# Performance work log

Measured on AMD Instinct MI355X. Metric: run time of the kernel, lower is better.

Reference implementation:

```python
import jax, jax.numpy as jnp
import numpy as np

B, N, K, H = 4, 2048, 30, 128
NODE_IN, EDGE_IN, FF = 21, 16, 4 * H


def _normalize(t, axis=-1):
    d = t / jnp.linalg.norm(t, axis=axis, keepdims=True)
    return jnp.where(jnp.isnan(d), 0.0, d)


def gather_nodes(nodes, idx):
    # nodes: [B,N,C], idx: [B,N,K] -> [B,N,K,C]
    b, n, k = idx.shape
    flat = idx.reshape(b, n * k)
    out = jnp.take_along_axis(nodes, flat[:, :, None], axis=1)
    return out.reshape(b, n, k, nodes.shape[-1])


def cal_dihedral(Xf, eps=1e-7):
    dX = Xf[:, 1:, :] - Xf[:, :-1, :]
    U = _normalize(dX)
    u0, u1, u2 = U[:, :-2], U[:, 1:-1], U[:, 2:]
    n0 = _normalize(jnp.cross(u0, u1))
    n1 = _normalize(jnp.cross(u1, u2))
    cosD = jnp.clip((n0 * n1).sum(-1), -1 + eps, 1 - eps)
    v = _normalize(jnp.cross(n0, n1))
    return jnp.sign((-v * u1).sum(-1)) * jnp.arccos(cosD)


def dihedrals(X, eps=1e-7):
    b, n = X.shape[0], X.shape[1]
    Xf = X[:, :, :3, :].reshape(b, 3 * n, 3)
    D = cal_dihedral(Xf)
    D = jnp.pad(D, ((0, 0), (1, 2))).reshape(b, n, 3)
    dihed = jnp.concatenate([jnp.cos(D), jnp.sin(D)], -1)
    dX = Xf[:, 1:] - Xf[:, :-1]
    U = _normalize(dX)
    cosA = jnp.clip((U[:, :-2] * U[:, 1:-1]).sum(-1), -1 + eps, 1 - eps)
    A = jnp.pad(jnp.arccos(cosA), ((0, 0), (1, 2))).reshape(b, n, 3)
    ang = jnp.concatenate([jnp.cos(A), jnp.sin(A)], -1)
    return jnp.concatenate([dihed, ang], -1)  # [B,N,12]


def quaternions(R):
    diag = jnp.diagonal(R, axis1=-2, axis2=-1)
    Rxx, Ryy, Rzz = diag[..., 0], diag[..., 1], diag[..., 2]
    mags = 0.5 * jnp.sqrt(jnp.abs(1 + jnp.stack([Rxx - Ryy - Rzz, -Rxx + Ryy - Rzz, -Rxx - Ryy + Rzz], -1)))
    signs = jnp.sign(jnp.stack([R[..., 2, 1] - R[..., 1, 2], R[..., 0, 2] - R[..., 2, 0], R[..., 1, 0] - R[..., 0, 1]], -1))
    xyz = signs * mags
    w = jnp.sqrt(jax.nn.relu(1 + diag.sum(-1, keepdims=True))) / 2.0
    return _normalize(jnp.concatenate([xyz, w], -1))


def orientations(X, E_idx):
    V = X  # [B,N,4,3]
    b, n = X.shape[0], X.shape[1]
    k = E_idx.shape[2]
    Xf = X[:, :, :3, :].reshape(b, 3 * n, 3)
    dX = Xf[:, 1:] - Xf[:, :-1]
    U = _normalize(dX)
    u0, u1 = U[:, :-2], U[:, 1:-1]
    n0 = _normalize(jnp.cross(u0, u1))[:, ::3]
    b1 = _normalize(u0 - u1)[:, ::3]
    Xa = Xf[:, ::3]  # [B,N,3]
    Q = jnp.stack([b1, n0, jnp.cross(b1, n0)], 2)  # [B,N-1,3,3]
    Q = Q.reshape(b, Q.shape[1], 9)
    Q = jnp.pad(Q, ((0, 0), (0, 1), (0, 0)))  # [B,N,9]
    Qn = gather_nodes(Q, E_idx).reshape(b, n, k, 3, 3)
    Xn = gather_nodes(V[:, :, 1, :], E_idx)
    Nn = gather_nodes(V[:, :, 0, :], E_idx)
    Cn = gather_nodes(V[:, :, 2, :], E_idx)
    On = gather_nodes(V[:, :, 3, :], E_idx)
    Q3 = Q.reshape(b, n, 3, 3)
    dXn = jnp.stack([Xn, Nn, Cn, On], 3) - Xa[:, :, None, None, :]  # [B,N,K,4,3]
    dU = jnp.einsum('bnij,bnkaj->bnkai', Q3, dXn)
    E_direct = _normalize(dU).reshape(b, n, k, 12)
    R = jnp.einsum('bnji,bnkjl->bnkil', Q3, Qn)  # Q^T @ Q_neighbors
    q = quaternions(R)  # [B,N,K,4]
    dX_inner = V[:, :, jnp.array([0, 2, 3]), :] - Xa[:, :, None, :]
    dU_inner = _normalize(jnp.einsum('bnij,bnaj->bnai', Q3, dX_inner))
    V_direct = dU_inner.reshape(b, n, 9)
    return V_direct, E_direct, q


def layernorm(x, g, bta, eps=1e-5):
    m = x.mean(-1, keepdims=True)
    v = ((x - m) ** 2).mean(-1, keepdims=True)
    return (x - m) / jnp.sqrt(v + eps) * g + bta


def gelu(x):
    return jax.nn.gelu(x, approximate=False)


def forward(X, E_idx, Wv_w, Wv_b, We_w, We_b, W1_w, W1_b, W2_w, W2_b, W3_w, W3_b,
            Wi_w, Wi_b, Wo_w, Wo_b, ln1_g, ln1_b, ln2_g, ln2_b):
    k = E_idx.shape[2]
    Dfeat = dihedrals(X)                     # [B,N,12]
    Vd, Ed, q = orientations(X, E_idx)       # [B,N,9],[B,N,K,12],[B,N,K,4]
    hV = jnp.concatenate([Dfeat, Vd], -1) @ Wv_w + Wv_b     # [B,N,H]
    hE = jnp.concatenate([Ed, q], -1) @ We_w + We_b         # [B,N,K,H]
    hV_nbr = gather_nodes(hV, E_idx)                        # [B,N,K,H]
    hV_exp = jnp.broadcast_to(hV[:, :, None, :], hV_nbr.shape)
    hEV = jnp.concatenate([hV_exp, hE, hV_nbr], -1)         # [B,N,K,3H]
    msg = gelu(hEV @ W1_w + W1_b)
    msg = gelu(msg @ W2_w + W2_b)
    msg = msg @ W3_w + W3_b
    dh = msg.sum(-2) / k
    hV = layernorm(hV + dh, ln1_g, ln1_b)
    ff = gelu(hV @ Wi_w + Wi_b) @ Wo_w + Wo_b
    hV = layernorm(hV + ff, ln2_g, ln2_b)
    return hV


def _lin(key, fan_in, fan_out):
    s = 1.0 / np.sqrt(fan_in)
    kw, kb = jax.random.split(key)
    return (jax.random.uniform(kw, (fan_in, fan_out), minval=-s, maxval=s),
            jax.random.uniform(kb, (fan_out,), minval=-s, maxval=s))


def setup_inputs() -> dict:
    key = jax.random.key(0)
    ks = jax.random.split(key, 10)
    X = jax.random.normal(ks[0], (B, N, 4, 3), dtype=jnp.float32) * 3.0
    E_idx = jax.random.randint(ks[1], (B, N, K), 0, N)
    Wv_w, Wv_b = _lin(ks[2], NODE_IN, H)
    We_w, We_b = _lin(ks[3], EDGE_IN, H)
    W1_w, W1_b = _lin(ks[4], 3 * H, H)
    W2_w, W2_b = _lin(ks[5], H, H)
    W3_w, W3_b = _lin(ks[6], H, H)
    Wi_w, Wi_b = _lin(ks[7], H, FF)
    Wo_w, Wo_b = _lin(ks[8], FF, H)
    return {
        'X': X, 'E_idx': E_idx,
        'Wv_w': Wv_w, 'Wv_b': Wv_b, 'We_w': We_w, 'We_b': We_b,
        'W1_w': W1_w, 'W1_b': W1_b, 'W2_w': W2_w, 'W2_b': W2_b,
        'W3_w': W3_w, 'W3_b': W3_b, 'Wi_w': Wi_w, 'Wi_b': Wi_b,
        'Wo_w': Wo_w, 'Wo_b': Wo_b,
        'ln1_g': jnp.ones((H,), jnp.float32), 'ln1_b': jnp.zeros((H,), jnp.float32),
        'ln2_g': jnp.ones((H,), jnp.float32), 'ln2_b': jnp.zeros((H,), jnp.float32),
    }


def reference(X, E_idx, Wv_w, Wv_b, We_w, We_b, W1_w, W1_b, W2_w, W2_b, W3_w, W3_b,
              Wi_w, Wi_b, Wo_w, Wo_b, ln1_g, ln1_b, ln2_g, ln2_b):
    return forward(X, E_idx, Wv_w, Wv_b, We_w, We_b, W1_w, W1_b, W2_w, W2_b,
                   W3_w, W3_b, Wi_w, Wi_b, Wo_w, Wo_b, ln1_g, ln1_b, ln2_g, ln2_b)
```

## Files before the change

kernel.cpp:

```cpp
#include <hip/hip_runtime.h>
#include <math.h>

#define BB 4
#define NN 2048
#define KNB 30
#define HH 128
#define FFD 512

typedef __attribute__((ext_vector_type(4))) float  f32x4;
typedef __attribute__((ext_vector_type(8))) short  s16x8;

struct F3 { float x,y,z; };
__device__ __forceinline__ F3 f3(float a,float b,float c){ F3 r; r.x=a; r.y=b; r.z=c; return r; }
__device__ __forceinline__ F3 sub3(F3 a, F3 b){ return f3(a.x-b.x, a.y-b.y, a.z-b.z); }
__device__ __forceinline__ float dot3(F3 a, F3 b){ return a.x*b.x + a.y*b.y + a.z*b.z; }
__device__ __forceinline__ F3 cross3(F3 a, F3 b){
  return f3(a.y*b.z-a.z*b.y, a.z*b.x-a.x*b.z, a.x*b.y-a.y*b.x);
}
__device__ __forceinline__ F3 nrm3(F3 a){
  float n2 = dot3(a,a);
  if (n2 <= 0.f) return f3(0.f,0.f,0.f);
  float inv = 1.0f/sqrtf(n2);
  return f3(a.x*inv, a.y*inv, a.z*inv);
}
__device__ __forceinline__ float sgnf(float x){ return (x>0.f)?1.f:((x<0.f)?-1.f:0.f); }
__device__ __forceinline__ float clip1(float x){
  const float e = 1e-7f;
  return fminf(fmaxf(x, -1.f+e), 1.f-e);
}
__device__ __forceinline__ float fgelu(float x){
  float u = 0.7978845608f*x*(1.f + 0.044715f*x*x);
  float d = 1.f + __builtin_amdgcn_exp2f(-2.8853900818f*u);
  return x * __builtin_amdgcn_rcpf(d);
}
__device__ __forceinline__ short f2bf(float x){
  union { float f; unsigned u; } v; v.f = x;
  unsigned r = v.u + 0x7fffu + ((v.u >> 16) & 1u);
  return (short)(r >> 16);
}

__global__ void k_geom(const float* __restrict__ X, float* __restrict__ Qws,
                       float* __restrict__ featws){
  int t = blockIdx.x*blockDim.x + threadIdx.x;
  if (t >= BB*NN) return;
  int b = t / NN, n = t % NN;
  const float* Xb = X + (size_t)b*NN*12;
  #define LD3(r,a) f3(Xb[((r)*4+(a))*3+0], Xb[((r)*4+(a))*3+1], Xb[((r)*4+(a))*3+2])
  F3 x0=LD3(n,0), x1=LD3(n,1), x2=LD3(n,2), x3=LD3(n,3);
  F3 U[5];
  U[1]=nrm3(sub3(x1,x0));
  U[2]=nrm3(sub3(x2,x1));
  if (n>0){ F3 p = LD3(n-1,2); U[0]=nrm3(sub3(x0,p)); } else U[0]=f3(0.f,0.f,0.f);
  if (n<NN-1){ F3 y0=LD3(n+1,0), y1=LD3(n+1,1); U[3]=nrm3(sub3(y0,x2)); U[4]=nrm3(sub3(y1,y0)); }
  else { U[3]=f3(0.f,0.f,0.f); U[4]=f3(0.f,0.f,0.f); }

  float feat[21];
  #pragma unroll
  for (int tt=0; tt<3; tt++){
    bool valid = (n>0 || tt>0) && (n<NN-1 || tt==0);
    if (valid){
      F3 a=U[tt], bv=U[tt+1], c=U[tt+2];
      F3 n0=nrm3(cross3(a,bv)), n1=nrm3(cross3(bv,c));
      float cd = clip1(dot3(n0,n1));
      F3 v = nrm3(cross3(n0,n1));
      float s = sgnf(-dot3(v,bv));
      feat[tt]   = (s==0.f) ? 1.f : cd;
      feat[3+tt] = s*sqrtf(fmaxf(1.f-cd*cd, 0.f));
      float ca = clip1(dot3(a,bv));
      feat[6+tt] = ca;
      feat[9+tt] = sqrtf(fmaxf(1.f-ca*ca, 0.f));
    } else {
      feat[tt]=1.f; feat[3+tt]=0.f; feat[6+tt]=1.f; feat[9+tt]=0.f;
    }
  }
  float Q[9];
  if (n<NN-1){
    F3 b1=nrm3(sub3(U[1],U[2]));
    F3 n0=nrm3(cross3(U[1],U[2]));
    F3 r2=cross3(b1,n0);
    Q[0]=b1.x;Q[1]=b1.y;Q[2]=b1.z;Q[3]=n0.x;Q[4]=n0.y;Q[5]=n0.z;Q[6]=r2.x;Q[7]=r2.y;Q[8]=r2.z;
  } else {
    #pragma unroll
    for (int i=0;i<9;i++) Q[i]=0.f;
  }
  float* qp = Qws + (size_t)t*9;
  #pragma unroll
  for (int i=0;i<9;i++) qp[i]=Q[i];

  feat[12]=0.f; feat[13]=0.f; feat[14]=0.f;
  F3 d1=sub3(x2,x0), d2=sub3(x3,x0);
  F3 r1 = nrm3(f3(Q[0]*d1.x+Q[1]*d1.y+Q[2]*d1.z,
                  Q[3]*d1.x+Q[4]*d1.y+Q[5]*d1.z,
                  Q[6]*d1.x+Q[7]*d1.y+Q[8]*d1.z));
  F3 r2v= nrm3(f3(Q[0]*d2.x+Q[1]*d2.y+Q[2]*d2.z,
                  Q[3]*d2.x+Q[4]*d2.y+Q[5]*d2.z,
                  Q[6]*d2.x+Q[7]*d2.y+Q[8]*d2.z));
  feat[15]=r1.x; feat[16]=r1.y; feat[17]=r1.z;
  feat[18]=r2v.x; feat[19]=r2v.y; feat[20]=r2v.z;
  float* fp = featws + (size_t)t*21;
  #pragma unroll
  for (int i=0;i<21;i++) fp[i]=feat[i];
  #undef LD3
}

__global__ void k_fold(const float* __restrict__ We, const float* __restrict__ Web,
                       const float* __restrict__ W1, const float* __restrict__ W2,
                       const float* __restrict__ Wi, const float* __restrict__ Wo,
                       float* __restrict__ Wfold, float* __restrict__ bfold,
                       short* __restrict__ w2t, short* __restrict__ w1aT,
                       short* __restrict__ w1cT, short* __restrict__ wiT,
                       short* __restrict__ woT){
  int t = blockIdx.x*256 + threadIdx.x;
  if (t < 2048){
    int j = t >> 7, c = t & 127;
    float a = 0.f;
    for (int k=0;k<HH;k++) a += We[j*HH+k]*W1[(HH+k)*HH + c];
    Wfold[t] = a;
  } else if (t < 2176){
    int c = t - 2048;
    float a = 0.f;
    for (int k=0;k<HH;k++) a += Web[k]*W1[(HH+k)*HH + c];
    bfold[c] = a;
  } else if (t < 18560){
    int i = t - 2176;  int n = i >> 7, k = i & 127;
    w2t[n*HH + k] = f2bf(W2[k*HH + n]);
  } else if (t < 34944){
    int i = t - 18560; int n = i >> 7, k = i & 127;
    w1aT[n*HH + k] = f2bf(W1[k*HH + n]);
  } else if (t < 51328){
    int i = t - 34944; int n = i >> 7, k = i & 127;
    w1cT[n*HH + k] = f2bf(W1[(256+k)*HH + n]);
  } else if (t < 116864){
    int i = t - 51328; int n = i >> 7, k = i & 127;
    wiT[n*HH + k] = f2bf(Wi[k*FFD + n]);
  } else if (t < 182400){
    int i = t - 116864; int k = i >> 7, n = i & 127;
    woT[n*FFD + k] = f2bf(Wo[k*HH + n]);
  }
}

#define PNB 32
__global__ void k_pre(const float* __restrict__ featws, const float* __restrict__ Wv,
                      const float* __restrict__ Wvb, const short* __restrict__ w1aT,
                      const short* __restrict__ w1cT, const float* __restrict__ W1b,
                      const float* __restrict__ bfold, float* __restrict__ hVws,
                      float* __restrict__ Sws, float* __restrict__ Gws){
  __shared__ __align__(16) short hvL[PNB][136];
  int tid = threadIdx.x;
  int base = blockIdx.x*PNB;
  {
    int c = tid & 127, half = tid >> 7;
    float wv[21];
    #pragma unroll
    for (int j=0;j<21;j++) wv[j] = Wv[j*HH + c];
    float wb = Wvb[c];
    #pragma unroll 2
    for (int it=0; it<16; ++it){
      int g = it*2 + half;
      const float* f = featws + (size_t)(base+g)*21;
      float a = wb;
      #pragma unroll
      for (int j=0;j<21;j++) a += f[j]*wv[j];
      hVws[(size_t)(base+g)*HH + c] = a;
      hvL[g][c] = f2bf(a);
    }
  }
  __syncthreads();
  {
    int l = tid & 63, w = tid >> 6;
    int lr = l & 15, lg = l >> 4;
    int m = w & 1;
    int nbase = (w >> 1)*4;
    s16x8 afr[4];
    #pragma unroll
    for (int ks=0; ks<4; ks++)
      afr[ks] = *reinterpret_cast<const s16x8*>(&hvL[m*16 + lr][ks*32 + lg*8]);
    f32x4 Cs[4], Cg[4];
    #pragma unroll
    for (int q=0;q<4;q++){ Cs[q]=(f32x4){0,0,0,0}; Cg[q]=(f32x4){0,0,0,0}; }
    #pragma unroll
    for (int q=0;q<4;q++){
      int ncol = (nbase+q)*16 + lr;
      #pragma unroll
      for (int ks=0; ks<4; ks++){
        s16x8 ba = *reinterpret_cast<const s16x8*>(&w1aT[ncol*HH + ks*32 + lg*8]);
        s16x8 bc = *reinterpret_cast<const s16x8*>(&w1cT[ncol*HH + ks*32 + lg*8]);
        Cs[q] = __builtin_amdgcn_mfma_f32_16x16x32_bf16(afr[ks], ba, Cs[q], 0,0,0);
        Cg[q] = __builtin_amdgcn_mfma_f32_16x16x32_bf16(afr[ks], bc, Cg[q], 0,0,0);
      }
    }
    #pragma unroll
    for (int q=0;q<4;q++){
      int ncol = (nbase+q)*16 + lr;
      float bc = W1b[ncol] + bfold[ncol];
      #pragma unroll
      for (int i=0;i<4;i++){
        int row = m*16 + lg*4 + i;
        size_t o = (size_t)(base+row)*HH + ncol;
        Sws[o] = Cs[q][i] + bc;
        Gws[o] = Cg[q][i];
      }
    }
  }
}

#define NPB 4
#define A2STR 136
__launch_bounds__(256, 3)
__global__ void k_msg(const float* __restrict__ X, const int* __restrict__ Eidx,
                      const float* __restrict__ Qws, const float* __restrict__ Sws,
                      const float* __restrict__ Gws, const float* __restrict__ hVws,
                      const float* __restrict__ Wfoldg, const short* __restrict__ w2t,
                      const float* __restrict__ W2b, const float* __restrict__ W3,
                      const float* __restrict__ W3b, float* __restrict__ xpre){
  __shared__ __align__(16) float efL[128*16];
  __shared__ int idxL[128];
  __shared__ __align__(16) short A2s[128*A2STR];
  __shared__ __align__(16) float csL[NPB*HH];

  const int tid = threadIdx.x;
  const int gbase = blockIdx.x*NPB;
  const int b = gbase >> 11;
  const int bofs = b*NN;

  if (tid < NPB*KNB){
    int nn = tid / KNB;
    int kk = tid - nn*KNB;
    int gnode = gbase + nn;
    int n = gnode - bofs;
    int j = Eidx[(size_t)gnode*KNB + kk];
    int r = nn*32 + kk;
    idxL[r] = j;
    const float* Qs = Qws + (size_t)gnode*9;
    float q[9];
    #pragma unroll
    for (int i=0;i<9;i++) q[i]=Qs[i];
    const float* Xb = X + (size_t)b*NN*12;
    F3 Xa = f3(Xb[n*12+0], Xb[n*12+1], Xb[n*12+2]);
    const float* Xn = Xb + (size_t)j*12;
    F3 A[4];
    A[0] = f3(Xn[3],  Xn[4],  Xn[5]);
    A[1] = f3(Xn[0],  Xn[1],  Xn[2]);
    A[2] = f3(Xn[6],  Xn[7],  Xn[8]);
    A[3] = f3(Xn[9],  Xn[10], Xn[11]);
    #pragma unroll
    for (int a=0;a<4;a++){
      F3 d = sub3(A[a], Xa);
      F3 w = f3(q[0]*d.x+q[1]*d.y+q[2]*d.z,
                q[3]*d.x+q[4]*d.y+q[5]*d.z,
                q[6]*d.x+q[7]*d.y+q[8]*d.z);
      F3 wn = nrm3(w);
      efL[r*16 + a*3 + 0] = wn.x;
      efL[r*16 + a*3 + 1] = wn.y;
      efL[r*16 + a*3 + 2] = wn.z;
    }
    const float* Qn = Qws + (size_t)(bofs + j)*9;
    float p[9];
    #pragma unroll
    for (int i=0;i<9;i++) p[i]=Qn[i];
    float R00=q[0]*p[0]+q[3]*p[3]+q[6]*p[6];
    float R01=q[0]*p[1]+q[3]*p[4]+q[6]*p[7];
    float R02=q[0]*p[2]+q[3]*p[5]+q[6]*p[8];
    float R10=q[1]*p[0]+q[4]*p[3]+q[7]*p[6];
    float R11=q[1]*p[1]+q[4]*p[4]+q[7]*p[7];
    float R12=q[1]*p[2]+q[4]*p[5]+q[7]*p[8];
    float R20=q[2]*p[0]+q[5]*p[3]+q[8]*p[6];
    float R21=q[2]*p[1]+q[5]*p[4]+q[8]*p[7];
    float R22=q[2]*p[2]+q[5]*p[5]+q[8]*p[8];
    float mx = 0.5f*sqrtf(fabsf(1.f+R00-R11-R22));
    float my = 0.5f*sqrtf(fabsf(1.f-R00+R11-R22));
    float mz = 0.5f*sqrtf(fabsf(1.f-R00-R11+R22));
    float qx = sgnf(R21-R12)*mx;
    float qy = sgnf(R02-R20)*my;
    float qz = sgnf(R10-R01)*mz;
    float qw = 0.5f*sqrtf(fmaxf(1.f+R00+R11+R22, 0.f));
    float n2 = qx*qx+qy*qy+qz*qz+qw*qw;
    float inv = (n2>0.f) ? 1.f/sqrtf(n2) : 0.f;
    efL[r*16+12]=qx*inv; efL[r*16+13]=qy*inv; efL[r*16+14]=qz*inv; efL[r*16+15]=qw*inv;
  }
  __syncthreads();

  {
    const int c  = tid & 127;
    const int rh = tid >> 7;
    float wf[16];
    #pragma unroll
    for (int j=0;j<16;j++) wf[j] = Wfoldg[j*HH + c];
    float Sv0 = Sws[(size_t)(gbase + rh*2    )*HH + c];
    float Sv1 = Sws[(size_t)(gbase + rh*2 + 1)*HH + c];
    #pragma unroll
    for (int r8=0; r8<8; r8++){
      int rbase = rh*64 + r8*8;
      float gv[8];
      #pragma unroll
      for (int u=0; u<8; u++){
        int r = rbase + u;
        int slot = r & 31;
        int nbr = idxL[r];
        gv[u] = (slot < KNB) ? Gws[(size_t)(bofs + nbr)*HH + c] : 0.f;
      }
      #pragma unroll
      for (int u=0; u<8; u++){
        int r = rbase + u;
        int slot = r & 31;
        short outv = 0;
        if (slot < KNB){
          const float4 e0 = *reinterpret_cast<const float4*>(&efL[r*16 + 0]);
          const float4 e1 = *reinterpret_cast<const float4*>(&efL[r*16 + 4]);
          const float4 e2 = *reinterpret_cast<const float4*>(&efL[r*16 + 8]);
          const float4 e3 = *reinterpret_cast<const float4*>(&efL[r*16 +12]);
          float acc = ((r>>5)&1) ? Sv1 : Sv0;
          acc += gv[u];
          acc += e0.x*wf[0] + e0.y*wf[1] + e0.z*wf[2] + e0.w*wf[3]
               + e1.x*wf[4] + e1.y*wf[5] + e1.z*wf[6] + e1.w*wf[7]
               + e2.x*wf[8] + e2.y*wf[9] + e2.z*wf[10]+ e2.w*wf[11]
               + e3.x*wf[12]+ e3.y*wf[13]+ e3.z*wf[14]+ e3.w*wf[15];
          outv = f2bf(fgelu(acc));
        }
        A2s[r*A2STR + c] = outv;
      }
    }
  }
  __syncthreads();

  {
    const int w  = tid >> 6;
    const int l  = tid & 63;
    const int lr = l & 15;
    const int lg = l >> 4;
    f32x4 Cacc[2][8];
    #pragma unroll
    for (int mt=0; mt<2; mt++)
      #pragma unroll
      for (int nt=0; nt<8; nt++)
        Cacc[mt][nt] = (f32x4){0.f,0.f,0.f,0.f};
    #pragma unroll
    for (int ks=0; ks<4; ks++){
      const int koff = ks*32 + lg*8;
      s16x8 a0 = *reinterpret_cast<const s16x8*>(&A2s[(w*32      + lr)*A2STR + koff]);
      s16x8 a1 = *reinterpret_cast<const s16x8*>(&A2s[(w*32 + 16 + lr)*A2STR + koff]);
      #pragma unroll
      for (int nt=0; nt<8; nt++){
        s16x8 bv = *reinterpret_cast<const s16x8*>(&w2t[(lr + nt*16)*HH + koff]);
        Cacc[0][nt] = __builtin_amdgcn_mfma_f32_16x16x32_bf16(a0, bv, Cacc[0][nt], 0,0,0);
        Cacc[1][nt] = __builtin_amdgcn_mfma_f32_16x16x32_bf16(a1, bv, Cacc[1][nt], 0,0,0);
      }
    }
    #pragma unroll
    for (int nt=0; nt<8; nt++){
      float b2v = W2b[lr + nt*16];
      float part = 0.f;
      #pragma unroll
      for (int mt=0; mt<2; mt++){
        #pragma unroll
        for (int i=0; i<4; i++){
          int row32 = mt*16 + lg*4 + i;
          float v = fgelu(Cacc[mt][nt][i] + b2v);
          if (row32 < KNB) part += v;
        }
      }
      part += __shfl_xor(part, 16, 64);
      part += __shfl_xor(part, 32, 64);
      if (l < 16) csL[w*HH + nt*16 + lr] = part;
    }
  }
  __syncthreads();

  {
    const int h = tid & 127;
    const int half = tid >> 7;
    #pragma unroll
    for (int q2=0; q2<2; q2++){
      int nn = half*2 + q2;
      const float* cs = csL + nn*HH;
      float acc = 0.f;
      for (int j=0;j<HH;j+=4){
        acc += cs[j]  *W3[(j  )*HH+h] + cs[j+1]*W3[(j+1)*HH+h]
             + cs[j+2]*W3[(j+2)*HH+h] + cs[j+3]*W3[(j+3)*HH+h];
      }
      size_t o = (size_t)(gbase + nn)*HH + h;
      xpre[o] = hVws[o] + acc*(1.f/30.f) + W3b[h];
    }
  }
}

#define FNB 16
__global__ void k_ffn(const float* __restrict__ xpre, const short* __restrict__ wiT,
                      const short* __restrict__ woT, const float* __restrict__ Wib,
                      const float* __restrict__ Wob, const float* __restrict__ l1g,
                      const float* __restrict__ l1b, const float* __restrict__ l2g,
                      const float* __restrict__ l2b, float* __restrict__ out){
  __shared__ __align__(16) short hv1[FNB][136];
  __shared__ __align__(16) float yL[FNB][HH];
  __shared__ __align__(16) short ffh[FNB][520];
  __shared__ float partS[FNB][4], partQ[FNB][4];
  const int tid = threadIdx.x;
  const int l = tid & 63, w = tid >> 6;
  const int base = blockIdx.x*FNB;

  #pragma unroll
  for (int ri=0; ri<4; ri++){
    int r = w*4 + ri;
    const float* xp = xpre + (size_t)(base+r)*HH;
    float x0 = xp[l], x1 = xp[l+64];
    float s = x0 + x1;
    #pragma unroll
    for (int o=32;o>0;o>>=1) s += __shfl_xor(s, o, 64);
    float mean = s*(1.f/HH);
    float d0 = x0-mean, d1 = x1-mean;
    float q = d0*d0 + d1*d1;
    #pragma unroll
    for (int o=32;o>0;o>>=1) q += __shfl_xor(q, o, 64);
    float inv = 1.f/sqrtf(q*(1.f/HH) + 1e-5f);
    float y0 = d0*inv*l1g[l]    + l1b[l];
    float y1 = d1*inv*l1g[l+64] + l1b[l+64];
    yL[r][l] = y0; yL[r][l+64] = y1;
    hv1[r][l] = f2bf(y0); hv1[r][l+64] = f2bf(y1);
  }
  __syncthreads();

  const int lr = l & 15, lg = l >> 4;
  {
    s16x8 afr[4];
    #pragma unroll
    for (int ks=0; ks<4; ks++)
      afr[ks] = *reinterpret_cast<const s16x8*>(&hv1[lr][ks*32 + lg*8]);
    #pragma unroll
    for (int q=0; q<8; q++){
      int ncol = (w*8+q)*16 + lr;
      f32x4 C = (f32x4){0,0,0,0};
      #pragma unroll
      for (int ks=0; ks<4; ks++){
        s16x8 bv = *reinterpret_cast<const s16x8*>(&wiT[ncol*HH + ks*32 + lg*8]);
        C = __builtin_amdgcn_mfma_f32_16x16x32_bf16(afr[ks], bv, C, 0,0,0);
      }
      float bi = Wib[ncol];
      #pragma unroll
      for (int i=0;i<4;i++){
        int row = lg*4 + i;
        ffh[row][ncol] = f2bf(fgelu(C[i] + bi));
      }
    }
  }
  __syncthreads();

  f32x4 C2[2];
  C2[0]=(f32x4){0,0,0,0}; C2[1]=(f32x4){0,0,0,0};
  for (int ks=0; ks<16; ++ks){
    s16x8 a = *reinterpret_cast<const s16x8*>(&ffh[lr][ks*32 + lg*8]);
    #pragma unroll
    for (int t2=0; t2<2; t2++){
      int ncol = (2*w+t2)*16 + lr;
      s16x8 bv = *reinterpret_cast<const s16x8*>(&woT[ncol*FFD + ks*32 + lg*8]);
      C2[t2] = __builtin_amdgcn_mfma_f32_16x16x32_bf16(a, bv, C2[t2], 0,0,0);
    }
  }
  float vv[2][4];
  float ps[4] = {0,0,0,0}, pq[4] = {0,0,0,0};
  #pragma unroll
  for (int t2=0; t2<2; t2++){
    int col = (2*w+t2)*16 + lr;
    float bo = Wob[col];
    #pragma unroll
    for (int i=0;i<4;i++){
      int row = lg*4 + i;
      float v = yL[row][col] + C2[t2][i] + bo;
      vv[t2][i] = v;
      ps[i] += v; pq[i] += v*v;
    }
  }
  #pragma unroll
  for (int i=0;i<4;i++){
    #pragma unroll
    for (int o=1;o<16;o<<=1){
      ps[i] += __shfl_xor(ps[i], o, 64);
      pq[i] += __shfl_xor(pq[i], o, 64);
    }
    if (lr == 0){ partS[lg*4+i][w] = ps[i]; partQ[lg*4+i][w] = pq[i]; }
  }
  __syncthreads();
  float mean[4], inv[4];
  #pragma unroll
  for (int i=0;i<4;i++){
    int row = lg*4 + i;
    float S = partS[row][0]+partS[row][1]+partS[row][2]+partS[row][3];
    float Q = partQ[row][0]+partQ[row][1]+partQ[row][2]+partQ[row][3];
    float m = S*(1.f/HH);
    float var = Q*(1.f/HH) - m*m;
    mean[i] = m;
    inv[i] = 1.f/sqrtf(var + 1e-5f);
  }
  #pragma unroll
  for (int t2=0; t2<2; t2++){
    int col = (2*w+t2)*16 + lr;
    float g2 = l2g[col], b2 = l2b[col];
    #pragma unroll
    for (int i=0;i<4;i++){
      int row = lg*4 + i;
      out[(size_t)(base+row)*HH + col] = (vv[t2][i]-mean[i])*inv[i]*g2 + b2;
    }
  }
}

extern "C" void kernel_launch(void* const* d_in, const int* in_sizes, int n_in,
                              void* d_out, int out_size, void* d_ws, size_t ws_size,
                              hipStream_t stream) {
  (void)in_sizes; (void)n_in; (void)out_size; (void)ws_size;
  const float* X   = (const float*)d_in[0];
  const int*   Ei  = (const int*)  d_in[1];
  const float* Wv  = (const float*)d_in[2];
  const float* Wvb = (const float*)d_in[3];
  const float* We  = (const float*)d_in[4];
  const float* Web = (const float*)d_in[5];
  const float* W1  = (const float*)d_in[6];
  const float* W1b = (const float*)d_in[7];
  const float* W2  = (const float*)d_in[8];
  const float* W2b = (const float*)d_in[9];
  const float* W3  = (const float*)d_in[10];
  const float* W3b = (const float*)d_in[11];
  const float* Wi  = (const float*)d_in[12];
  const float* Wib = (const float*)d_in[13];
  const float* Wo  = (const float*)d_in[14];
  const float* Wob = (const float*)d_in[15];
  const float* l1g = (const float*)d_in[16];
  const float* l1b = (const float*)d_in[17];
  const float* l2g = (const float*)d_in[18];
  const float* l2b = (const float*)d_in[19];
  float* out = (float*)d_out;

  float* wsf    = (float*)d_ws;
  float* featws = wsf + 0;
  float* Qws    = wsf + 172032;
  float* hVws   = wsf + 245760;
  float* Gws    = wsf + 1294336;
  float* Sws    = wsf + 2342912;
  float* xprews = Sws;
  float* Wfold  = wsf + 3391488;
  float* bfold  = wsf + 3393536;
  short* w2t    = (short*)(wsf + 3393664);
  short* w1aT   = (short*)(wsf + 3401856);
  short* w1cT   = (short*)(wsf + 3410048);
  short* wiT    = (short*)(wsf + 3418240);
  short* woT    = (short*)(wsf + 3451008);

  k_geom<<<dim3(64),   dim3(128), 0, stream>>>(X, Qws, featws);
  k_fold<<<dim3(713),  dim3(256), 0, stream>>>(We, Web, W1, W2, Wi, Wo,
                                               Wfold, bfold, w2t, w1aT, w1cT, wiT, woT);
  k_pre <<<dim3(BB*NN/PNB), dim3(256), 0, stream>>>(featws, Wv, Wvb, w1aT, w1cT,
                                                    W1b, bfold, hVws, Sws, Gws);
  k_msg <<<dim3(BB*NN/NPB), dim3(256), 0, stream>>>(X, Ei, Qws, Sws, Gws, hVws,
                                                    Wfold, w2t, W2b, W3, W3b, xprews);
  k_ffn <<<dim3(BB*NN/FNB), dim3(256), 0, stream>>>(xprews, wiT, woT, Wib, Wob,
                                                    l1g, l1b, l2g, l2b, out);
}
```

Measured before the change: 212.9 us.

## Use MFMA for edge-feature fold in k_msg and merge geometry/fold kernels

The per-edge 16-wide edge-feature projection in k_msg moves from scalar FMAs to bf16 MFMA, with edge features and the folded weight stored as bf16 in a padded LDS layout. The csL buffer now aliases efL, which shrinks LDS use, and launch bounds rise to 4 blocks per SM. k_geom and k_fold are merged into one launch to save a kernel launch, and the GELU polynomial is refactored into fewer operations. Edge features are quantized to bf16, which costs some accuracy. The Gws gathers are now per-MFMA-lane and may coalesce less well.

```diff
diff --git a/kernel.cpp b/kernel.cpp
--- a/kernel.cpp
+++ b/kernel.cpp
@@ -9,6 +9,7 @@
 
 typedef __attribute__((ext_vector_type(4))) float  f32x4;
 typedef __attribute__((ext_vector_type(8))) short  s16x8;
+typedef __attribute__((ext_vector_type(4))) short  s16x4;
 
 struct F3 { float x,y,z; };
 __device__ __forceinline__ F3 f3(float a,float b,float c){ F3 r; r.x=a; r.y=b; r.z=c; return r; }
@@ -29,8 +30,9 @@
   return fminf(fmaxf(x, -1.f+e), 1.f-e);
 }
 __device__ __forceinline__ float fgelu(float x){
-  float u = 0.7978845608f*x*(1.f + 0.044715f*x*x);
-  float d = 1.f + __builtin_amdgcn_exp2f(-2.8853900818f*u);
+  float x2 = x*x;
+  float t = __builtin_fmaf(-0.1029641763f, x2, -2.302344055f);
+  float d = 1.f + __builtin_amdgcn_exp2f(t*x);
   return x * __builtin_amdgcn_rcpf(d);
 }
 __device__ __forceinline__ short f2bf(float x){
@@ -39,83 +41,83 @@
   return (short)(r >> 16);
 }
 
-__global__ void k_geom(const float* __restrict__ X, float* __restrict__ Qws,
-                       float* __restrict__ featws){
-  int t = blockIdx.x*blockDim.x + threadIdx.x;
-  if (t >= BB*NN) return;
-  int b = t / NN, n = t % NN;
-  const float* Xb = X + (size_t)b*NN*12;
-  #define LD3(r,a) f3(Xb[((r)*4+(a))*3+0], Xb[((r)*4+(a))*3+1], Xb[((r)*4+(a))*3+2])
-  F3 x0=LD3(n,0), x1=LD3(n,1), x2=LD3(n,2), x3=LD3(n,3);
-  F3 U[5];
-  U[1]=nrm3(sub3(x1,x0));
-  U[2]=nrm3(sub3(x2,x1));
-  if (n>0){ F3 p = LD3(n-1,2); U[0]=nrm3(sub3(x0,p)); } else U[0]=f3(0.f,0.f,0.f);
-  if (n<NN-1){ F3 y0=LD3(n+1,0), y1=LD3(n+1,1); U[3]=nrm3(sub3(y0,x2)); U[4]=nrm3(sub3(y1,y0)); }
-  else { U[3]=f3(0.f,0.f,0.f); U[4]=f3(0.f,0.f,0.f); }
-
-  float feat[21];
-  #pragma unroll
-  for (int tt=0; tt<3; tt++){
-    bool valid = (n>0 || tt>0) && (n<NN-1 || tt==0);
-    if (valid){
-      F3 a=U[tt], bv=U[tt+1], c=U[tt+2];
-      F3 n0=nrm3(cross3(a,bv)), n1=nrm3(cross3(bv,c));
-      float cd = clip1(dot3(n0,n1));
-      F3 v = nrm3(cross3(n0,n1));
-      float s = sgnf(-dot3(v,bv));
-      feat[tt]   = (s==0.f) ? 1.f : cd;
-      feat[3+tt] = s*sqrtf(fmaxf(1.f-cd*cd, 0.f));
-      float ca = clip1(dot3(a,bv));
-      feat[6+tt] = ca;
-      feat[9+tt] = sqrtf(fmaxf(1.f-ca*ca, 0.f));
-    } else {
-      feat[tt]=1.f; feat[3+tt]=0.f; feat[6+tt]=1.f; feat[9+tt]=0.f;
-    }
-  }
-  float Q[9];
-  if (n<NN-1){
-    F3 b1=nrm3(sub3(U[1],U[2]));
-    F3 n0=nrm3(cross3(U[1],U[2]));
-    F3 r2=cross3(b1,n0);
-    Q[0]=b1.x;Q[1]=b1.y;Q[2]=b1.z;Q[3]=n0.x;Q[4]=n0.y;Q[5]=n0.z;Q[6]=r2.x;Q[7]=r2.y;Q[8]=r2.z;
-  } else {
-    #pragma unroll
-    for (int i=0;i<9;i++) Q[i]=0.f;
-  }
-  float* qp = Qws + (size_t)t*9;
-  #pragma unroll
-  for (int i=0;i<9;i++) qp[i]=Q[i];
-
-  feat[12]=0.f; feat[13]=0.f; feat[14]=0.f;
-  F3 d1=sub3(x2,x0), d2=sub3(x3,x0);
-  F3 r1 = nrm3(f3(Q[0]*d1.x+Q[1]*d1.y+Q[2]*d1.z,
-                  Q[3]*d1.x+Q[4]*d1.y+Q[5]*d1.z,
-                  Q[6]*d1.x+Q[7]*d1.y+Q[8]*d1.z));
-  F3 r2v= nrm3(f3(Q[0]*d2.x+Q[1]*d2.y+Q[2]*d2.z,
-                  Q[3]*d2.x+Q[4]*d2.y+Q[5]*d2.z,
-                  Q[6]*d2.x+Q[7]*d2.y+Q[8]*d2.z));
-  feat[15]=r1.x; feat[16]=r1.y; feat[17]=r1.z;
-  feat[18]=r2v.x; feat[19]=r2v.y; feat[20]=r2v.z;
-  float* fp = featws + (size_t)t*21;
-  #pragma unroll
-  for (int i=0;i<21;i++) fp[i]=feat[i];
-  #undef LD3
-}
-
-__global__ void k_fold(const float* __restrict__ We, const float* __restrict__ Web,
+__global__ void k_init(const float* __restrict__ X, float* __restrict__ Qws,
+                       float* __restrict__ featws,
+                       const float* __restrict__ We, const float* __restrict__ Web,
                        const float* __restrict__ W1, const float* __restrict__ W2,
                        const float* __restrict__ Wi, const float* __restrict__ Wo,
-                       float* __restrict__ Wfold, float* __restrict__ bfold,
+                       short* __restrict__ wfoldT, float* __restrict__ bfold,
                        short* __restrict__ w2t, short* __restrict__ w1aT,
                        short* __restrict__ w1cT, short* __restrict__ wiT,
                        short* __restrict__ woT){
-  int t = blockIdx.x*256 + threadIdx.x;
+  if (blockIdx.x < 32){
+    int t = blockIdx.x*256 + threadIdx.x;
+    int b = t / NN, n = t % NN;
+    const float* Xb = X + (size_t)b*NN*12;
+    #define LD3(r,a) f3(Xb[((r)*4+(a))*3+0], Xb[((r)*4+(a))*3+1], Xb[((r)*4+(a))*3+2])
+    F3 x0=LD3(n,0), x1=LD3(n,1), x2=LD3(n,2), x3=LD3(n,3);
+    F3 U[5];
+    U[1]=nrm3(sub3(x1,x0));
+    U[2]=nrm3(sub3(x2,x1));
+    if (n>0){ F3 p = LD3(n-1,2); U[0]=nrm3(sub3(x0,p)); } else U[0]=f3(0.f,0.f,0.f);
+    if (n<NN-1){ F3 y0=LD3(n+1,0), y1=LD3(n+1,1); U[3]=nrm3(sub3(y0,x2)); U[4]=nrm3(sub3(y1,y0)); }
+    else { U[3]=f3(0.f,0.f,0.f); U[4]=f3(0.f,0.f,0.f); }
+
+    float feat[21];
+    #pragma unroll
+    for (int tt=0; tt<3; tt++){
+      bool valid = (n>0 || tt>0) && (n<NN-1 || tt==0);
+      if (valid){
+        F3 a=U[tt], bv=U[tt+1], c=U[tt+2];
+        F3 n0=nrm3(cross3(a,bv)), n1=nrm3(cross3(bv,c));
+        float cd = clip1(dot3(n0,n1));
+        F3 v = nrm3(cross3(n0,n1));
+        float s = sgnf(-dot3(v,bv));
+        feat[tt]   = (s==0.f) ? 1.f : cd;
+        feat[3+tt] = s*sqrtf(fmaxf(1.f-cd*cd, 0.f));
+        float ca = clip1(dot3(a,bv));
+        feat[6+tt] = ca;
+        feat[9+tt] = sqrtf(fmaxf(1.f-ca*ca, 0.f));
+      } else {
+        feat[tt]=1.f; feat[3+tt]=0.f; feat[6+tt]=1.f; feat[9+tt]=0.f;
+      }
+    }
+    float Q[9];
+    if (n<NN-1){
+      F3 b1=nrm3(sub3(U[1],U[2]));
+      F3 n0=nrm3(cross3(U[1],U[2]));
+      F3 r2=cross3(b1,n0);
+      Q[0]=b1.x;Q[1]=b1.y;Q[2]=b1.z;Q[3]=n0.x;Q[4]=n0.y;Q[5]=n0.z;Q[6]=r2.x;Q[7]=r2.y;Q[8]=r2.z;
+    } else {
+      #pragma unroll
+      for (int i=0;i<9;i++) Q[i]=0.f;
+    }
+    float* qp = Qws + (size_t)t*9;
+    #pragma unroll
+    for (int i=0;i<9;i++) qp[i]=Q[i];
+
+    feat[12]=0.f; feat[13]=0.f; feat[14]=0.f;
+    F3 d1=sub3(x2,x0), d2=sub3(x3,x0);
+    F3 r1 = nrm3(f3(Q[0]*d1.x+Q[1]*d1.y+Q[2]*d1.z,
+                    Q[3]*d1.x+Q[4]*d1.y+Q[5]*d1.z,
+                    Q[6]*d1.x+Q[7]*d1.y+Q[8]*d1.z));
+    F3 r2v= nrm3(f3(Q[0]*d2.x+Q[1]*d2.y+Q[2]*d2.z,
+                    Q[3]*d2.x+Q[4]*d2.y+Q[5]*d2.z,
+                    Q[6]*d2.x+Q[7]*d2.y+Q[8]*d2.z));
+    feat[15]=r1.x; feat[16]=r1.y; feat[17]=r1.z;
+    feat[18]=r2v.x; feat[19]=r2v.y; feat[20]=r2v.z;
+    float* fp = featws + (size_t)t*21;
+    #pragma unroll
+    for (int i=0;i<21;i++) fp[i]=feat[i];
+    #undef LD3
+    return;
+  }
+  int t = (blockIdx.x-32)*256 + threadIdx.x;
   if (t < 2048){
-    int j = t >> 7, c = t & 127;
+    int c = t >> 4, j = t & 15;
     float a = 0.f;
     for (int k=0;k<HH;k++) a += We[j*HH+k]*W1[(HH+k)*HH + c];
-    Wfold[t] = a;
+    wfoldT[t] = f2bf(a);
   } else if (t < 2176){
     int c = t - 2048;
     float a = 0.f;
@@ -206,17 +208,18 @@
 
 #define NPB 4
 #define A2STR 136
-__launch_bounds__(256, 3)
+#define EFSTR 20
+__launch_bounds__(256, 4)
 __global__ void k_msg(const float* __restrict__ X, const int* __restrict__ Eidx,
                       const float* __restrict__ Qws, const float* __restrict__ Sws,
                       const float* __restrict__ Gws, const float* __restrict__ hVws,
-                      const float* __restrict__ Wfoldg, const short* __restrict__ w2t,
+                      const short* __restrict__ wfoldT, const short* __restrict__ w2t,
                       const float* __restrict__ W2b, const float* __restrict__ W3,
                       const float* __restrict__ W3b, float* __restrict__ xpre){
-  __shared__ __align__(16) float efL[128*16];
+  __shared__ __align__(16) short efL[128*EFSTR];
   __shared__ int idxL[128];
   __shared__ __align__(16) short A2s[128*A2STR];
-  __shared__ __align__(16) float csL[NPB*HH];
+  float* csL = (float*)efL;
 
   const int tid = threadIdx.x;
   const int gbase = blockIdx.x*NPB;
@@ -250,9 +253,9 @@
                 q[3]*d.x+q[4]*d.y+q[5]*d.z,
                 q[6]*d.x+q[7]*d.y+q[8]*d.z);
       F3 wn = nrm3(w);
-      efL[r*16 + a*3 + 0] = wn.x;
-      efL[r*16 + a*3 + 1] = wn.y;
-      efL[r*16 + a*3 + 2] = wn.z;
+      efL[r*EFSTR + a*3 + 0] = f2bf(wn.x);
+      efL[r*EFSTR + a*3 + 1] = f2bf(wn.y);
+      efL[r*EFSTR + a*3 + 2] = f2bf(wn.z);
     }
     const float* Qn = Qws + (size_t)(bofs + j)*9;
     float p[9];
@@ -276,58 +279,75 @@
     float qw = 0.5f*sqrtf(fmaxf(1.f+R00+R11+R22, 0.f));
     float n2 = qx*qx+qy*qy+qz*qz+qw*qw;
     float inv = (n2>0.f) ? 1.f/sqrtf(n2) : 0.f;
-    efL[r*16+12]=qx*inv; efL[r*16+13]=qy*inv; efL[r*16+14]=qz*inv; efL[r*16+15]=qw*inv;
-  }
-  __syncthreads();
+    efL[r*EFSTR+12]=f2bf(qx*inv); efL[r*EFSTR+13]=f2bf(qy*inv);
+    efL[r*EFSTR+14]=f2bf(qz*inv); efL[r*EFSTR+15]=f2bf(qw*inv);
+  } else if (tid < 128){
+    int e = tid - 120;
+    int nn = e >> 1, slot = 30 + (e & 1);
+    int r = nn*32 + slot;
+    idxL[r] = 0;
+    #pragma unroll
+    for (int j2=0;j2<16;j2++) efL[r*EFSTR + j2] = 0;
+  }
+  __syncthreads();
+
+  const int w  = tid >> 6;
+  const int l  = tid & 63;
+  const int lr = l & 15;
+  const int lg = l >> 4;
 
   {
-    const int c  = tid & 127;
-    const int rh = tid >> 7;
-    float wf[16];
-    #pragma unroll
-    for (int j=0;j<16;j++) wf[j] = Wfoldg[j*HH + c];
-    float Sv0 = Sws[(size_t)(gbase + rh*2    )*HH + c];
-    float Sv1 = Sws[(size_t)(gbase + rh*2 + 1)*HH + c];
-    #pragma unroll
-    for (int r8=0; r8<8; r8++){
-      int rbase = rh*64 + r8*8;
-      float gv[8];
-      #pragma unroll
-      for (int u=0; u<8; u++){
-        int r = rbase + u;
-        int slot = r & 31;
-        int nbr = idxL[r];
-        gv[u] = (slot < KNB) ? Gws[(size_t)(bofs + nbr)*HH + c] : 0.f;
-      }
-      #pragma unroll
-      for (int u=0; u<8; u++){
-        int r = rbase + u;
-        int slot = r & 31;
-        short outv = 0;
-        if (slot < KNB){
-          const float4 e0 = *reinterpret_cast<const float4*>(&efL[r*16 + 0]);
-          const float4 e1 = *reinterpret_cast<const float4*>(&efL[r*16 + 4]);
-          const float4 e2 = *reinterpret_cast<const float4*>(&efL[r*16 + 8]);
-          const float4 e3 = *reinterpret_cast<const float4*>(&efL[r*16 +12]);
-          float acc = ((r>>5)&1) ? Sv1 : Sv0;
-          acc += gv[u];
-          acc += e0.x*wf[0] + e0.y*wf[1] + e0.z*wf[2] + e0.w*wf[3]
-               + e1.x*wf[4] + e1.y*wf[5] + e1.z*wf[6] + e1.w*wf[7]
-               + e2.x*wf[8] + e2.y*wf[9] + e2.z*wf[10]+ e2.w*wf[11]
-               + e3.x*wf[12]+ e3.y*wf[13]+ e3.z*wf[14]+ e3.w*wf[15];
-          outv = f2bf(fgelu(acc));
+    s16x8 bf[8];
+    #pragma unroll
+    for (int ct=0; ct<8; ct++){
+      if (lg < 2)
+        bf[ct] = *reinterpret_cast<const s16x8*>(&wfoldT[(ct*16+lr)*16 + lg*8]);
+      else
+        bf[ct] = (s16x8){0,0,0,0,0,0,0,0};
+    }
+    s16x8 af[2];
+    #pragma unroll
+    for (int rt=0; rt<2; rt++){
+      if (lg < 2){
+        const short* p = &efL[(w*32 + rt*16 + lr)*EFSTR + lg*8];
+        s16x4 lo = *reinterpret_cast<const s16x4*>(p);
+        s16x4 hi = *reinterpret_cast<const s16x4*>(p+4);
+        s16x8 v;
+        #pragma unroll
+        for (int j2=0;j2<4;j2++){ v[j2]=lo[j2]; v[4+j2]=hi[j2]; }
+        af[rt] = v;
+      } else {
+        af[rt] = (s16x8){0,0,0,0,0,0,0,0};
+      }
+    }
+    int goff[2][4];
+    #pragma unroll
+    for (int rt=0; rt<2; rt++)
+      #pragma unroll
+      for (int i=0;i<4;i++)
+        goff[rt][i] = (bofs + idxL[w*32 + rt*16 + lg*4 + i])*HH;
+
+    const float* Srow = Sws + (size_t)(gbase+w)*HH;
+    #pragma unroll
+    for (int ct=0; ct<8; ct++){
+      int col = ct*16 + lr;
+      float sv = Srow[col];
+      #pragma unroll
+      for (int rt=0; rt<2; rt++){
+        f32x4 C = __builtin_amdgcn_mfma_f32_16x16x32_bf16(af[rt], bf[ct], (f32x4){0,0,0,0}, 0,0,0);
+        #pragma unroll
+        for (int i=0;i<4;i++){
+          int slot = rt*16 + lg*4 + i;
+          float g = Gws[goff[rt][i] + col];
+          float v = (slot < KNB) ? fgelu(C[i] + sv + g) : 0.f;
+          A2s[(w*32 + slot)*A2STR + col] = f2bf(v);
         }
-        A2s[r*A2STR + c] = outv;
       }
     }
   }
   __syncthreads();
 
   {
-    const int w  = tid >> 6;
-    const int l  = tid & 63;
-    const int lr = l & 15;
-    const int lg = l >> 4;
     f32x4 Cacc[2][8];
     #pragma unroll
     for (int mt=0; mt<2; mt++)
@@ -535,21 +555,20 @@
   float* Gws    = wsf + 1294336;
   float* Sws    = wsf + 2342912;
   float* xprews = Sws;
-  float* Wfold  = wsf + 3391488;
-  float* bfold  = wsf + 3393536;
-  short* w2t    = (short*)(wsf + 3393664);
-  short* w1aT   = (short*)(wsf + 3401856);
-  short* w1cT   = (short*)(wsf + 3410048);
-  short* wiT    = (short*)(wsf + 3418240);
-  short* woT    = (short*)(wsf + 3451008);
-
-  k_geom<<<dim3(64),   dim3(128), 0, stream>>>(X, Qws, featws);
-  k_fold<<<dim3(713),  dim3(256), 0, stream>>>(We, Web, W1, W2, Wi, Wo,
-                                               Wfold, bfold, w2t, w1aT, w1cT, wiT, woT);
+  short* wfoldT = (short*)(wsf + 3391488);
+  float* bfold  = wsf + 3392512;
+  short* w2t    = (short*)(wsf + 3392640);
+  short* w1aT   = (short*)(wsf + 3400832);
+  short* w1cT   = (short*)(wsf + 3409024);
+  short* wiT    = (short*)(wsf + 3417216);
+  short* woT    = (short*)(wsf + 3449984);
+
+  k_init<<<dim3(745), dim3(256), 0, stream>>>(X, Qws, featws, We, Web, W1, W2, Wi, Wo,
+                                              wfoldT, bfold, w2t, w1aT, w1cT, wiT, woT);
   k_pre <<<dim3(BB*NN/PNB), dim3(256), 0, stream>>>(featws, Wv, Wvb, w1aT, w1cT,
                                                     W1b, bfold, hVws, Sws, Gws);
   k_msg <<<dim3(BB*NN/NPB), dim3(256), 0, stream>>>(X, Ei, Qws, Sws, Gws, hVws,
-                                                    Wfold, w2t, W2b, W3, W3b, xprews);
+                                                    wfoldT, w2t, W2b, W3, W3b, xprews);
   k_ffn <<<dim3(BB*NN/FNB), dim3(256), 0, stream>>>(xprews, wiT, woT, Wib, Wob,
                                                     l1g, l1b, l2g, l2b, out);
 }
```

Result: faster. 202.5 us (-4.9%).
